# Performance work log

Measured on AMD Instinct MI355X. Metric: run time of the kernel, lower is better.

## Reference

```python
import jax, jax.numpy as jnp
import numpy as np

B, T, DD, NS, V, E, H, L = 8192, 200, 8, 4, 1000, 32, 256, 2


def setup_inputs() -> dict:
    key = jax.random.key(0)
    ks = jax.random.split(key, 10)
    s = 0.05
    dense = jax.random.normal(ks[0], (B, T, DD), jnp.float32)
    sparse = jax.random.randint(ks[1], (B, T, NS), 0, V)
    lengths = jax.random.randint(ks[2], (B,), 1, T + 1)
    emb_tables = jax.random.normal(ks[3], (NS, V, E), jnp.float32) * s
    Wl = jax.random.normal(ks[4], (H, DD + NS * E), jnp.float32) * s
    bl = jnp.zeros((H,), jnp.float32)
    # axis1: 0 = rnn_entry_exit (even t), 1 = rnn_exit_entry (odd t)
    Wih = jax.random.normal(ks[5], (L, 2, H, H), jnp.float32) * s
    Whh = jax.random.normal(ks[6], (L, 2, H, H), jnp.float32) * s
    bih = jnp.zeros((L, 2, H), jnp.float32)
    bhh = jnp.zeros((L, 2, H), jnp.float32)
    Wout = jax.random.normal(ks[7], (1, H), jnp.float32) * s
    bout = jnp.zeros((1,), jnp.float32)
    return dict(dense=dense, sparse=sparse, lengths=lengths, emb_tables=emb_tables,
                Wl=Wl, bl=bl, Wih=Wih, Whh=Whh, bih=bih, bhh=bhh, Wout=Wout, bout=bout)


def reference(dense, sparse, lengths, emb_tables, Wl, bl, Wih, Whh, bih, bhh, Wout, bout):
    # Padded+mask formulation; equivalent to the packed-sequence loop:
    # finished sequences' hidden states are frozen (== being sliced away),
    # and the final frozen h of the top layer is the per-sequence output.
    # Dropout is identity (eval mode); it is never applied in forward anyway.
    mask = jnp.arange(T)[None, :] < lengths[:, None]        # [B, T]
    d_t = jnp.swapaxes(dense, 0, 1)                          # [T, B, DD]
    s_t = jnp.swapaxes(sparse, 0, 1)                         # [T, B, NS]
    m_t = mask.T                                             # [T, B]

    def embed(st):  # [B, NS] -> [B, NS*E], matching torch.cat of per-feature embeddings
        e = jax.vmap(lambda tab, idx: tab[idx], in_axes=(0, 1), out_axes=1)(emb_tables, st)
        return e.reshape(st.shape[0], NS * E)

    def step(h, xs):  # h: [L, B, H]
        t, dt, st, mt = xs
        x = jnp.concatenate([dt, embed(st)], axis=-1)        # [B, DD+NS*E]
        x = jax.nn.relu(x @ Wl.T + bl)                       # [B, H]
        p = t % 2                                            # which cell set this step
        hs = []
        for i in range(L):
            hn = jnp.tanh(x @ Wih[i, p].T + bih[i, p] + h[i] @ Whh[i, p].T + bhh[i, p])
            hi = jnp.where(mt[:, None], hn, h[i])
            hs.append(hi)
            x = hi
        return jnp.stack(hs), None

    h0 = jnp.zeros((L, B, H), dense.dtype)
    hT, _ = jax.lax.scan(step, h0, (jnp.arange(T), d_t, s_t, m_t))
    return jax.nn.sigmoid(hT[-1] @ Wout.T + bout)[:, 0]     # [B]
```

## Files before the change

kernel.cpp:

```cpp
#include <hip/hip_runtime.h>
#include <math.h>


typedef __attribute__((ext_vector_type(8))) short bf16x8;
typedef __attribute__((ext_vector_type(4))) short s16x4;
typedef __attribute__((ext_vector_type(4))) float f32x4;

#define MFMA(a, b, c) __builtin_amdgcn_mfma_f32_16x16x32_bf16((a), (b), (c), 0, 0, 0)

#define T_  200

#define WLP_OFF   0
#define WIHP_OFF  40960
#define WHHP_OFF  (40960 + 262144)
#define BSUM_BYTE_OFF ((40960 + 262144 + 262144) * 2)

#define XCS 168
#define HS  264
#define SM_XCAT 0
#define SM_XPJ  5376
#define SM_H0   (SM_XPJ + 8448)
#define SM_H1A  (SM_H0 + 8448)
#define SM_H1B  (SM_H1A + 8448)
#define SM_BIAS (SM_H1B + 8448)
#define SM_TOT  (SM_BIAS + 2560)

__device__ __forceinline__ short f2bf(float f) {
    unsigned u = __float_as_uint(f);
    u += 0x7fffu + ((u >> 16) & 1u);
    return (short)(u >> 16);
}
__device__ __forceinline__ float bf2f(short s) {
    return __uint_as_float(((unsigned)(unsigned short)s) << 16);
}
__device__ __forceinline__ float tanh_fast(float x) {
    float e = __builtin_amdgcn_exp2f(x * 2.88539008f);
    return 1.0f - 2.0f * __builtin_amdgcn_rcpf(e + 1.0f);
}

__global__ void prep_kernel(const float* __restrict__ Wl,
                            const float* __restrict__ Wih,
                            const float* __restrict__ Whh,
                            const float* __restrict__ bih,
                            const float* __restrict__ bhh,
                            short* __restrict__ wsS,
                            float* __restrict__ bsum) {
    int tid = blockIdx.x * 256 + threadIdx.x;
    if (tid < 5120) {
        int mt = tid / 320, rem = tid % 320;
        int kk = rem / 64, lane = rem % 64;
        int o = mt * 16 + (lane & 15);
        int kb = kk * 32 + (lane >> 4) * 8;
        short* dst = wsS + WLP_OFF + tid * 8;
#pragma unroll
        for (int e = 0; e < 8; e++) {
            int k = kb + e;
            dst[e] = f2bf((k < 136) ? Wl[o * 136 + k] : 0.0f);
        }
    } else if (tid < 5120 + 32768) {
        int jj = tid - 5120;
        int mat = jj / 8192, rem = jj % 8192;
        int lane = rem & 63, kk = (rem >> 6) & 7, mt = rem >> 9;
        int o = mt * 16 + (lane & 15);
        int kb = kk * 32 + (lane >> 4) * 8;
        const float* src = Wih + (mat * 256 + o) * 256;
        short* dst = wsS + WIHP_OFF + mat * 65536 + rem * 8;
#pragma unroll
        for (int e = 0; e < 8; e++) dst[e] = f2bf(src[kb + e]);
    } else if (tid < 5120 + 65536) {
        int jj = tid - 37888;
        int mat = jj / 8192, rem = jj % 8192;
        int lane = rem & 63, kk = (rem >> 6) & 7, mt = rem >> 9;
        int o = mt * 16 + (lane & 15);
        int kb = kk * 32 + (lane >> 4) * 8;
        const float* src = Whh + (mat * 256 + o) * 256;
        short* dst = wsS + WHHP_OFF + mat * 65536 + rem * 8;
#pragma unroll
        for (int e = 0; e < 8; e++) dst[e] = f2bf(src[kb + e]);
    } else if (tid < 5120 + 65536 + 1024) {
        int j = tid - 70656;
        bsum[j] = bih[j] + bhh[j];
    }
}

struct GReg { f32x4 e0, e1, dv; };

__device__ __forceinline__ void gather_load(GReg& g, const float* __restrict__ dense,
                                            const int* __restrict__ sparse,
                                            const float* __restrict__ emb,
                                            int b0, int tt, int tid) {
    int gs = tid >> 4, gf = (tid >> 2) & 3, gq = tid & 3;
    int ix = sparse[(b0 + gs) * (T_ * 4) + tt * 4 + gf];
    const float* ep = emb + gf * 32000 + ix * 32 + gq * 8;
    g.e0 = *(const f32x4*)ep;
    g.e1 = *(const f32x4*)(ep + 4);
    if (tid < 64)
        g.dv = *(const f32x4*)(dense + (b0 + (tid >> 1)) * (T_ * 8) + tt * 8 + (tid & 1) * 4);
}
__device__ __forceinline__ void gather_commit(const GReg& g, short* __restrict__ buf, int tid) {
    int gs = tid >> 4, gf = (tid >> 2) & 3, gq = tid & 3;
    s16x4 w0, w1;
#pragma unroll
    for (int r = 0; r < 4; r++) { w0[r] = f2bf(g.e0[r]); w1[r] = f2bf(g.e1[r]); }
    int off = gs * XCS + 8 + gf * 32 + gq * 8;
    *(s16x4*)(buf + off) = w0;
    *(s16x4*)(buf + off + 4) = w1;
    if (tid < 64) {
        s16x4 wd;
#pragma unroll
        for (int r = 0; r < 4; r++) wd[r] = f2bf(g.dv[r]);
        *(s16x4*)(buf + (tid >> 1) * XCS + (tid & 1) * 4) = wd;
    }
}

__device__ __forceinline__ void phaseA(const short* __restrict__ xcat,
                                       short* __restrict__ xpj,
                                       const short* __restrict__ Wlp,
                                       const float* __restrict__ blS,
                                       int lane, int lrow, int lgrp, int wid) {
    bf16x8 wl[3][2];
#pragma unroll
    for (int j = 0; j < 2; j++) {
        wl[j][0] = *(const bf16x8*)(Wlp + (((wid * 2 + 0) * 5 + j) * 64 + lane) * 8);
        wl[j][1] = *(const bf16x8*)(Wlp + (((wid * 2 + 1) * 5 + j) * 64 + lane) * 8);
    }
    f32x4 xacc[2][2];
#pragma unroll
    for (int mt = 0; mt < 2; mt++) {
        f32x4 bi = *(const f32x4*)(blS + wid * 32 + mt * 16 + lgrp * 4);
        xacc[mt][0] = bi; xacc[mt][1] = bi;
    }
#pragma unroll
    for (int kk = 0; kk < 5; kk++) {
        const int cur = kk % 3;
        if (kk < 3) {
            const int nxt = (kk + 2) % 3;
            wl[nxt][0] = *(const bf16x8*)(Wlp + (((wid * 2 + 0) * 5 + kk + 2) * 64 + lane) * 8);
            wl[nxt][1] = *(const bf16x8*)(Wlp + (((wid * 2 + 1) * 5 + kk + 2) * 64 + lane) * 8);
        }
        bf16x8 bxf[2];
#pragma unroll
        for (int nt = 0; nt < 2; nt++)
            bxf[nt] = *(const bf16x8*)(xcat + (nt * 16 + lrow) * XCS + kk * 32 + lgrp * 8);
#pragma unroll
        for (int mt = 0; mt < 2; mt++)
#pragma unroll
            for (int nt = 0; nt < 2; nt++) xacc[mt][nt] = MFMA(wl[cur][mt], bxf[nt], xacc[mt][nt]);
    }
#pragma unroll
    for (int mt = 0; mt < 2; mt++) {
        int o0 = wid * 32 + mt * 16 + lgrp * 4;
#pragma unroll
        for (int nt = 0; nt < 2; nt++) {
            s16x4 w;
#pragma unroll
            for (int r = 0; r < 4; r++) w[r] = f2bf(fmaxf(xacc[mt][nt][r], 0.0f));
            *(s16x4*)(xpj + (nt * 16 + lrow) * HS + o0) = w;
        }
    }
}

__global__ __launch_bounds__(512, 1) void rnn_kernel(
    const float* __restrict__ dense, const int* __restrict__ sparse,
    const int* __restrict__ lengths, const float* __restrict__ emb,
    const float* __restrict__ bl, const float* __restrict__ Wout,
    const float* __restrict__ bout, const short* __restrict__ wsS,
    const float* __restrict__ bsum, float* __restrict__ out) {
    __shared__ alignas(16) short sm[SM_TOT];
    short* xcat = sm + SM_XCAT;
    short* xpj  = sm + SM_XPJ;
    short* h0p  = sm + SM_H0;
    short* h1a  = sm + SM_H1A;
    short* h1b  = sm + SM_H1B;
    float* blS  = (float*)(sm + SM_BIAS);

    const int tid  = threadIdx.x;
    const int wid  = tid >> 6;
    const int lane = tid & 63;
    const int lrow = lane & 15;
    const int lgrp = lane >> 4;
    const int b0   = blockIdx.x * 32;
    const short* Wlp = wsS + WLP_OFF;

    for (int i = tid; i < SM_BIAS; i += 512) sm[i] = 0;
    for (int i = tid; i < 1280; i += 512)
        blS[i] = (i < 256) ? bl[i] : bsum[i - 256];

    const int len0 = lengths[b0 + lrow];
    const int len1 = lengths[b0 + 16 + lrow];

    __syncthreads();
    { GReg g0; gather_load(g0, dense, sparse, emb, b0, 0, tid); gather_commit(g0, xcat, tid); }
    __syncthreads();
    phaseA(xcat, xpj, Wlp, blS, lane, lrow, lgrp, wid);

    bf16x8 hreg0[2][8];
#pragma unroll
    for (int nt = 0; nt < 2; nt++)
#pragma unroll
        for (int kk = 0; kk < 8; kk++) {
            bf16x8 z;
#pragma unroll
            for (int e = 0; e < 8; e++) z[e] = 0;
            hreg0[nt][kk] = z;
        }
    __syncthreads();

    for (int t = 0; t < T_; t++) {
        const int p = t & 1;
        const bool hasNext = (t + 1 < T_);
        const short* Aih1 = wsS + WIHP_OFF + p * 65536;
        const short* Ahh1 = wsS + WHHP_OFF + p * 65536;
        const short* Aih2 = wsS + WIHP_OFF + (2 + p) * 65536;
        const short* Ahh2 = wsS + WHHP_OFF + (2 + p) * 65536;

        GReg g;
        if (hasNext) gather_load(g, dense, sparse, emb, b0, t + 1, tid);

        {
            bf16x8 wa[3][4];
#pragma unroll
            for (int j = 0; j < 2; j++) {
                wa[j][0] = *(const bf16x8*)(Aih1 + (((wid * 2 + 0) * 8 + j) * 64 + lane) * 8);
                wa[j][1] = *(const bf16x8*)(Aih1 + (((wid * 2 + 1) * 8 + j) * 64 + lane) * 8);
                wa[j][2] = *(const bf16x8*)(Ahh1 + (((wid * 2 + 0) * 8 + j) * 64 + lane) * 8);
                wa[j][3] = *(const bf16x8*)(Ahh1 + (((wid * 2 + 1) * 8 + j) * 64 + lane) * 8);
            }
            f32x4 acc[2][2];
#pragma unroll
            for (int mt = 0; mt < 2; mt++) {
                f32x4 bi = *(const f32x4*)(blS + 256 + p * 256 + wid * 32 + mt * 16 + lgrp * 4);
                acc[mt][0] = bi; acc[mt][1] = bi;
            }
#pragma unroll
            for (int kk = 0; kk < 8; kk++) {
                const int cur = kk % 3;
                if (kk < 6) {
                    const int nxt = (kk + 2) % 3;
                    wa[nxt][0] = *(const bf16x8*)(Aih1 + (((wid * 2 + 0) * 8 + kk + 2) * 64 + lane) * 8);
                    wa[nxt][1] = *(const bf16x8*)(Aih1 + (((wid * 2 + 1) * 8 + kk + 2) * 64 + lane) * 8);
                    wa[nxt][2] = *(const bf16x8*)(Ahh1 + (((wid * 2 + 0) * 8 + kk + 2) * 64 + lane) * 8);
                    wa[nxt][3] = *(const bf16x8*)(Ahh1 + (((wid * 2 + 1) * 8 + kk + 2) * 64 + lane) * 8);
                }
                bf16x8 bxf[2];
#pragma unroll
                for (int nt = 0; nt < 2; nt++)
                    bxf[nt] = *(const bf16x8*)(xpj + (nt * 16 + lrow) * HS + kk * 32 + lgrp * 8);
#pragma unroll
                for (int mt = 0; mt < 2; mt++)
#pragma unroll
                    for (int nt = 0; nt < 2; nt++) {
                        acc[mt][nt] = MFMA(wa[cur][mt], bxf[nt], acc[mt][nt]);
                        acc[mt][nt] = MFMA(wa[cur][2 + mt], hreg0[nt][kk], acc[mt][nt]);
                    }
            }
#pragma unroll
            for (int mt = 0; mt < 2; mt++) {
                int o0 = wid * 32 + mt * 16 + lgrp * 4;
#pragma unroll
                for (int nt = 0; nt < 2; nt++) {
                    s16x4 w;
#pragma unroll
                    for (int r = 0; r < 4; r++) w[r] = f2bf(tanh_fast(acc[mt][nt][r]));
                    int len = nt ? len1 : len0;
                    if (t < len)
                        *(s16x4*)(h0p + (nt * 16 + lrow) * HS + o0) = w;
                }
            }
        }
        if (hasNext) gather_commit(g, xcat, tid);
        __syncthreads();

        {
            const short* h1r = p ? h1b : h1a;
            short* h1w = p ? h1a : h1b;

            bf16x8 wa[3][4];
#pragma unroll
            for (int j = 0; j < 2; j++) {
                wa[j][0] = *(const bf16x8*)(Aih2 + (((wid * 2 + 0) * 8 + j) * 64 + lane) * 8);
                wa[j][1] = *(const bf16x8*)(Aih2 + (((wid * 2 + 1) * 8 + j) * 64 + lane) * 8);
                wa[j][2] = *(const bf16x8*)(Ahh2 + (((wid * 2 + 0) * 8 + j) * 64 + lane) * 8);
                wa[j][3] = *(const bf16x8*)(Ahh2 + (((wid * 2 + 1) * 8 + j) * 64 + lane) * 8);
            }
            f32x4 acc[2][2];
#pragma unroll
            for (int mt = 0; mt < 2; mt++) {
                f32x4 bi = *(const f32x4*)(blS + 256 + (2 + p) * 256 + wid * 32 + mt * 16 + lgrp * 4);
                acc[mt][0] = bi; acc[mt][1] = bi;
            }
#pragma unroll
            for (int kk = 0; kk < 8; kk++) {
                const int cur = kk % 3;
                if (kk < 6) {
                    const int nxt = (kk + 2) % 3;
                    wa[nxt][0] = *(const bf16x8*)(Aih2 + (((wid * 2 + 0) * 8 + kk + 2) * 64 + lane) * 8);
                    wa[nxt][1] = *(const bf16x8*)(Aih2 + (((wid * 2 + 1) * 8 + kk + 2) * 64 + lane) * 8);
                    wa[nxt][2] = *(const bf16x8*)(Ahh2 + (((wid * 2 + 0) * 8 + kk + 2) * 64 + lane) * 8);
                    wa[nxt][3] = *(const bf16x8*)(Ahh2 + (((wid * 2 + 1) * 8 + kk + 2) * 64 + lane) * 8);
                }
                bf16x8 bhf[2];
#pragma unroll
                for (int nt = 0; nt < 2; nt++) {
                    hreg0[nt][kk] = *(const bf16x8*)(h0p + (nt * 16 + lrow) * HS + kk * 32 + lgrp * 8);
                    bhf[nt] = *(const bf16x8*)(h1r + (nt * 16 + lrow) * HS + kk * 32 + lgrp * 8);
                }
#pragma unroll
                for (int mt = 0; mt < 2; mt++)
#pragma unroll
                    for (int nt = 0; nt < 2; nt++) {
                        acc[mt][nt] = MFMA(wa[cur][mt], hreg0[nt][kk], acc[mt][nt]);
                        acc[mt][nt] = MFMA(wa[cur][2 + mt], bhf[nt], acc[mt][nt]);
                    }
            }

            if (hasNext)
                phaseA(xcat, xpj, Wlp, blS, lane, lrow, lgrp, wid);

#pragma unroll
            for (int mt = 0; mt < 2; mt++) {
                int o0 = wid * 32 + mt * 16 + lgrp * 4;
#pragma unroll
                for (int nt = 0; nt < 2; nt++) {
                    int roff = (nt * 16 + lrow) * HS + o0;
                    s16x4 oldv = *(const s16x4*)(h1r + roff);
                    s16x4 w;
#pragma unroll
                    for (int r = 0; r < 4; r++) w[r] = f2bf(tanh_fast(acc[mt][nt][r]));
                    int len = nt ? len1 : len0;
                    *(s16x4*)(h1w + roff) = (t < len) ? w : oldv;
                }
            }
        }
        __syncthreads();
    }

    float* red = (float*)(sm + SM_XPJ);
    if (tid < 256) {
        int s = tid >> 3, part = tid & 7;
        const short* hr = h1a + s * HS + part * 32;
        float sum = 0.0f;
#pragma unroll
        for (int k = 0; k < 32; k++) sum += bf2f(hr[k]) * Wout[part * 32 + k];
        red[s * 8 + part] = sum;
    }
    __syncthreads();
    if (tid < 32) {
        float x = bout[0];
#pragma unroll
        for (int i = 0; i < 8; i++) x += red[tid * 8 + i];
        float e = __builtin_amdgcn_exp2f(x * 1.44269504f);
        out[b0 + tid] = 1.0f - __builtin_amdgcn_rcpf(1.0f + e);
    }
}

extern "C" void kernel_launch(void* const* d_in, const int* in_sizes, int n_in,
                              void* d_out, int out_size, void* d_ws, size_t ws_size,
                              hipStream_t stream) {
    const float* dense   = (const float*)d_in[0];
    const int*   sparse  = (const int*)d_in[1];
    const int*   lengths = (const int*)d_in[2];
    const float* emb     = (const float*)d_in[3];
    const float* Wl      = (const float*)d_in[4];
    const float* bl      = (const float*)d_in[5];
    const float* Wih     = (const float*)d_in[6];
    const float* Whh     = (const float*)d_in[7];
    const float* bih     = (const float*)d_in[8];
    const float* bhh     = (const float*)d_in[9];
    const float* Wout    = (const float*)d_in[10];
    const float* bout    = (const float*)d_in[11];

    short* wsS  = (short*)d_ws;
    float* bsum = (float*)((char*)d_ws + BSUM_BYTE_OFF);

    prep_kernel<<<280, 256, 0, stream>>>(Wl, Wih, Whh, bih, bhh, wsS, bsum);
    rnn_kernel<<<256, 512, 0, stream>>>(dense, sparse, lengths, emb, bl, Wout, bout,
                                        wsS, bsum, (float*)d_out);
}
```

Before: 1.205 ms.

## Software-pipeline weight loads across RNN layers and steps with rotating register slots

Restructures each time step into a template function whose weight-fragment loads run three chunks ahead in a 4-slot rotating register buffer, continuing across layer-1, layer-2, the next step's input projection, and the next step's layer-1 weights. The loop is unrolled by 4 so slot offsets are compile-time constants. The input projection moves after the layer-2 output write, and barriers become explicit lgkmcnt waits plus s_barrier with a sched_barrier. The goal is to hide the global/L2 weight-load latency at layer and step boundaries, at the cost of more register pressure and a longer unrolled body.

```diff
diff --git a/kernel.cpp b/kernel.cpp
--- a/kernel.cpp
+++ b/kernel.cpp
@@ -24,6 +24,10 @@
 #define SM_H1B  (SM_H1A + 8448)
 #define SM_BIAS (SM_H1B + 8448)
 #define SM_TOT  (SM_BIAS + 2560)
+
+#define LGKM0()    asm volatile("s_waitcnt lgkmcnt(0)" ::: "memory")
+#define BARRIER()  do { LGKM0(); __builtin_amdgcn_s_barrier(); \
+                        __builtin_amdgcn_sched_barrier(0); } while (0)
 
 __device__ __forceinline__ short f2bf(float f) {
     unsigned u = __float_as_uint(f);
@@ -113,39 +117,69 @@
     }
 }
 
-__device__ __forceinline__ void phaseA(const short* __restrict__ xcat,
-                                       short* __restrict__ xpj,
-                                       const short* __restrict__ Wlp,
-                                       const float* __restrict__ blS,
-                                       int lane, int lrow, int lgrp, int wid) {
-    bf16x8 wl[3][2];
-#pragma unroll
-    for (int j = 0; j < 2; j++) {
-        wl[j][0] = *(const bf16x8*)(Wlp + (((wid * 2 + 0) * 5 + j) * 64 + lane) * 8);
-        wl[j][1] = *(const bf16x8*)(Wlp + (((wid * 2 + 1) * 5 + j) * 64 + lane) * 8);
-    }
-    f32x4 xacc[2][2];
+__device__ __forceinline__ void load_chunk(bf16x8 (&wa)[4][4], int slot,
+                                           const short* A, const short* B,
+                                           int kk, int wid, int lane) {
+    wa[slot][0] = *(const bf16x8*)(A + (((wid * 2 + 0) * 8 + kk) * 64 + lane) * 8);
+    wa[slot][1] = *(const bf16x8*)(A + (((wid * 2 + 1) * 8 + kk) * 64 + lane) * 8);
+    wa[slot][2] = *(const bf16x8*)(B + (((wid * 2 + 0) * 8 + kk) * 64 + lane) * 8);
+    wa[slot][3] = *(const bf16x8*)(B + (((wid * 2 + 1) * 8 + kk) * 64 + lane) * 8);
+}
+__device__ __forceinline__ void load_wl(bf16x8 (&wa)[4][4], int slot,
+                                        const short* Wlp, int kk, int wid, int lane) {
+    wa[slot][0] = *(const bf16x8*)(Wlp + (((wid * 2 + 0) * 5 + kk) * 64 + lane) * 8);
+    wa[slot][1] = *(const bf16x8*)(Wlp + (((wid * 2 + 1) * 5 + kk) * 64 + lane) * 8);
+}
+
+template<int P, int OFF, bool LAST>
+__device__ __forceinline__ void rnn_step(
+    int t,
+    const float* __restrict__ dense, const int* __restrict__ sparse,
+    const float* __restrict__ emb, const short* __restrict__ wsS,
+    const float* __restrict__ blS,
+    short* __restrict__ xcat, short* __restrict__ xpj, short* __restrict__ h0p,
+    short* __restrict__ h1a, short* __restrict__ h1b,
+    bf16x8 (&wa)[4][4], bf16x8 (&hreg0)[2][8],
+    int lane, int lrow, int lgrp, int wid, int len0, int len1, int b0, int tid)
+{
+    const short* Aih1 = wsS + WIHP_OFF + P * 65536;
+    const short* Ahh1 = wsS + WHHP_OFF + P * 65536;
+    const short* Aih2 = wsS + WIHP_OFF + (2 + P) * 65536;
+    const short* Ahh2 = wsS + WHHP_OFF + (2 + P) * 65536;
+    const short* AihN = wsS + WIHP_OFF + (P ^ 1) * 65536;
+    const short* AhhN = wsS + WHHP_OFF + (P ^ 1) * 65536;
+    const short* Wlp  = wsS + WLP_OFF;
+
+    GReg g;
+    if (!LAST) gather_load(g, dense, sparse, emb, b0, t + 1, tid);
+
+    f32x4 acc[2][2];
+
 #pragma unroll
     for (int mt = 0; mt < 2; mt++) {
-        f32x4 bi = *(const f32x4*)(blS + wid * 32 + mt * 16 + lgrp * 4);
-        xacc[mt][0] = bi; xacc[mt][1] = bi;
-    }
-#pragma unroll
-    for (int kk = 0; kk < 5; kk++) {
-        const int cur = kk % 3;
-        if (kk < 3) {
-            const int nxt = (kk + 2) % 3;
-            wl[nxt][0] = *(const bf16x8*)(Wlp + (((wid * 2 + 0) * 5 + kk + 2) * 64 + lane) * 8);
-            wl[nxt][1] = *(const bf16x8*)(Wlp + (((wid * 2 + 1) * 5 + kk + 2) * 64 + lane) * 8);
-        }
+        f32x4 bi = *(const f32x4*)(blS + 256 + P * 256 + wid * 32 + mt * 16 + lgrp * 4);
+        acc[mt][0] = bi; acc[mt][1] = bi;
+    }
+#pragma unroll
+    for (int u = 0; u < 8; u++) {
+        {
+            const int v = u + 3;
+            const int vs = (v + OFF) & 3;
+            if (v < 8) load_chunk(wa, vs, Aih1, Ahh1, v, wid, lane);
+            else       load_chunk(wa, vs, Aih2, Ahh2, v - 8, wid, lane);
+        }
+        const int slot = (u + OFF) & 3;
         bf16x8 bxf[2];
 #pragma unroll
         for (int nt = 0; nt < 2; nt++)
-            bxf[nt] = *(const bf16x8*)(xcat + (nt * 16 + lrow) * XCS + kk * 32 + lgrp * 8);
+            bxf[nt] = *(const bf16x8*)(xpj + (nt * 16 + lrow) * HS + u * 32 + lgrp * 8);
 #pragma unroll
         for (int mt = 0; mt < 2; mt++)
 #pragma unroll
-            for (int nt = 0; nt < 2; nt++) xacc[mt][nt] = MFMA(wl[cur][mt], bxf[nt], xacc[mt][nt]);
+            for (int nt = 0; nt < 2; nt++) {
+                acc[mt][nt] = MFMA(wa[slot][mt], bxf[nt], acc[mt][nt]);
+                acc[mt][nt] = MFMA(wa[slot][2 + mt], hreg0[nt][u], acc[mt][nt]);
+            }
     }
 #pragma unroll
     for (int mt = 0; mt < 2; mt++) {
@@ -154,10 +188,100 @@
         for (int nt = 0; nt < 2; nt++) {
             s16x4 w;
 #pragma unroll
-            for (int r = 0; r < 4; r++) w[r] = f2bf(fmaxf(xacc[mt][nt][r], 0.0f));
-            *(s16x4*)(xpj + (nt * 16 + lrow) * HS + o0) = w;
-        }
-    }
+            for (int r = 0; r < 4; r++) w[r] = f2bf(tanh_fast(acc[mt][nt][r]));
+            int len = nt ? len1 : len0;
+            if (t < len)
+                *(s16x4*)(h0p + (nt * 16 + lrow) * HS + o0) = w;
+        }
+    }
+    if (!LAST) gather_commit(g, xcat, tid);
+    BARRIER();
+
+    const short* h1r = P ? h1b : h1a;
+    short* h1w = P ? h1a : h1b;
+#pragma unroll
+    for (int mt = 0; mt < 2; mt++) {
+        f32x4 bi = *(const f32x4*)(blS + 256 + (2 + P) * 256 + wid * 32 + mt * 16 + lgrp * 4);
+        acc[mt][0] = bi; acc[mt][1] = bi;
+    }
+#pragma unroll
+    for (int u = 8; u < 16; u++) {
+        {
+            const int v = u + 3;
+            const int vs = (v + OFF) & 3;
+            if (v < 16)      load_chunk(wa, vs, Aih2, Ahh2, v - 8, wid, lane);
+            else if (!LAST)  load_wl(wa, vs, Wlp, v - 16, wid, lane);
+        }
+        const int slot = (u + OFF) & 3;
+        const int kk = u - 8;
+        bf16x8 bhf[2];
+#pragma unroll
+        for (int nt = 0; nt < 2; nt++) {
+            hreg0[nt][kk] = *(const bf16x8*)(h0p + (nt * 16 + lrow) * HS + kk * 32 + lgrp * 8);
+            bhf[nt] = *(const bf16x8*)(h1r + (nt * 16 + lrow) * HS + kk * 32 + lgrp * 8);
+        }
+#pragma unroll
+        for (int mt = 0; mt < 2; mt++)
+#pragma unroll
+            for (int nt = 0; nt < 2; nt++) {
+                acc[mt][nt] = MFMA(wa[slot][mt], hreg0[nt][kk], acc[mt][nt]);
+                acc[mt][nt] = MFMA(wa[slot][2 + mt], bhf[nt], acc[mt][nt]);
+            }
+    }
+#pragma unroll
+    for (int mt = 0; mt < 2; mt++) {
+        int o0 = wid * 32 + mt * 16 + lgrp * 4;
+#pragma unroll
+        for (int nt = 0; nt < 2; nt++) {
+            int roff = (nt * 16 + lrow) * HS + o0;
+            s16x4 oldv = *(const s16x4*)(h1r + roff);
+            s16x4 w;
+#pragma unroll
+            for (int r = 0; r < 4; r++) w[r] = f2bf(tanh_fast(acc[mt][nt][r]));
+            int len = nt ? len1 : len0;
+            *(s16x4*)(h1w + roff) = (t < len) ? w : oldv;
+        }
+    }
+
+    if (!LAST) {
+#pragma unroll
+        for (int mt = 0; mt < 2; mt++) {
+            f32x4 bi = *(const f32x4*)(blS + wid * 32 + mt * 16 + lgrp * 4);
+            acc[mt][0] = bi; acc[mt][1] = bi;
+        }
+#pragma unroll
+        for (int u = 16; u < 21; u++) {
+            {
+                const int v = u + 3;
+                const int vs = (v + OFF) & 3;
+                if (v < 21) load_wl(wa, vs, Wlp, v - 16, wid, lane);
+                else        load_chunk(wa, vs, AihN, AhhN, v - 21, wid, lane);
+            }
+            const int slot = (u + OFF) & 3;
+            const int kk = u - 16;
+            bf16x8 bxf[2];
+#pragma unroll
+            for (int nt = 0; nt < 2; nt++)
+                bxf[nt] = *(const bf16x8*)(xcat + (nt * 16 + lrow) * XCS + kk * 32 + lgrp * 8);
+#pragma unroll
+            for (int mt = 0; mt < 2; mt++)
+#pragma unroll
+                for (int nt = 0; nt < 2; nt++)
+                    acc[mt][nt] = MFMA(wa[slot][mt], bxf[nt], acc[mt][nt]);
+        }
+#pragma unroll
+        for (int mt = 0; mt < 2; mt++) {
+            int o0 = wid * 32 + mt * 16 + lgrp * 4;
+#pragma unroll
+            for (int nt = 0; nt < 2; nt++) {
+                s16x4 w;
+#pragma unroll
+                for (int r = 0; r < 4; r++) w[r] = f2bf(fmaxf(acc[mt][nt][r], 0.0f));
+                *(s16x4*)(xpj + (nt * 16 + lrow) * HS + o0) = w;
+            }
+        }
+    }
+    BARRIER();
 }
 
 __global__ __launch_bounds__(512, 1) void rnn_kernel(
@@ -192,8 +316,42 @@
     __syncthreads();
     { GReg g0; gather_load(g0, dense, sparse, emb, b0, 0, tid); gather_commit(g0, xcat, tid); }
     __syncthreads();
-    phaseA(xcat, xpj, Wlp, blS, lane, lrow, lgrp, wid);
-
+
+    {
+        f32x4 xacc[2][2];
+#pragma unroll
+        for (int mt = 0; mt < 2; mt++) {
+            f32x4 bi = *(const f32x4*)(blS + wid * 32 + mt * 16 + lgrp * 4);
+            xacc[mt][0] = bi; xacc[mt][1] = bi;
+        }
+#pragma unroll
+        for (int kk = 0; kk < 5; kk++) {
+            bf16x8 wl0 = *(const bf16x8*)(Wlp + (((wid * 2 + 0) * 5 + kk) * 64 + lane) * 8);
+            bf16x8 wl1 = *(const bf16x8*)(Wlp + (((wid * 2 + 1) * 5 + kk) * 64 + lane) * 8);
+            bf16x8 bxf[2];
+#pragma unroll
+            for (int nt = 0; nt < 2; nt++)
+                bxf[nt] = *(const bf16x8*)(xcat + (nt * 16 + lrow) * XCS + kk * 32 + lgrp * 8);
+#pragma unroll
+            for (int nt = 0; nt < 2; nt++) {
+                xacc[0][nt] = MFMA(wl0, bxf[nt], xacc[0][nt]);
+                xacc[1][nt] = MFMA(wl1, bxf[nt], xacc[1][nt]);
+            }
+        }
+#pragma unroll
+        for (int mt = 0; mt < 2; mt++) {
+            int o0 = wid * 32 + mt * 16 + lgrp * 4;
+#pragma unroll
+            for (int nt = 0; nt < 2; nt++) {
+                s16x4 w;
+#pragma unroll
+                for (int r = 0; r < 4; r++) w[r] = f2bf(fmaxf(xacc[mt][nt][r], 0.0f));
+                *(s16x4*)(xpj + (nt * 16 + lrow) * HS + o0) = w;
+            }
+        }
+    }
+
+    bf16x8 wa[4][4];
     bf16x8 hreg0[2][8];
 #pragma unroll
     for (int nt = 0; nt < 2; nt++)
@@ -204,136 +362,28 @@
             for (int e = 0; e < 8; e++) z[e] = 0;
             hreg0[nt][kk] = z;
         }
-    __syncthreads();
-
-    for (int t = 0; t < T_; t++) {
-        const int p = t & 1;
-        const bool hasNext = (t + 1 < T_);
-        const short* Aih1 = wsS + WIHP_OFF + p * 65536;
-        const short* Ahh1 = wsS + WHHP_OFF + p * 65536;
-        const short* Aih2 = wsS + WIHP_OFF + (2 + p) * 65536;
-        const short* Ahh2 = wsS + WHHP_OFF + (2 + p) * 65536;
-
-        GReg g;
-        if (hasNext) gather_load(g, dense, sparse, emb, b0, t + 1, tid);
-
-        {
-            bf16x8 wa[3][4];
-#pragma unroll
-            for (int j = 0; j < 2; j++) {
-                wa[j][0] = *(const bf16x8*)(Aih1 + (((wid * 2 + 0) * 8 + j) * 64 + lane) * 8);
-                wa[j][1] = *(const bf16x8*)(Aih1 + (((wid * 2 + 1) * 8 + j) * 64 + lane) * 8);
-                wa[j][2] = *(const bf16x8*)(Ahh1 + (((wid * 2 + 0) * 8 + j) * 64 + lane) * 8);
-                wa[j][3] = *(const bf16x8*)(Ahh1 + (((wid * 2 + 1) * 8 + j) * 64 + lane) * 8);
-            }
-            f32x4 acc[2][2];
-#pragma unroll
-            for (int mt = 0; mt < 2; mt++) {
-                f32x4 bi = *(const f32x4*)(blS + 256 + p * 256 + wid * 32 + mt * 16 + lgrp * 4);
-                acc[mt][0] = bi; acc[mt][1] = bi;
-            }
-#pragma unroll
-            for (int kk = 0; kk < 8; kk++) {
-                const int cur = kk % 3;
-                if (kk < 6) {
-                    const int nxt = (kk + 2) % 3;
-                    wa[nxt][0] = *(const bf16x8*)(Aih1 + (((wid * 2 + 0) * 8 + kk + 2) * 64 + lane) * 8);
-                    wa[nxt][1] = *(const bf16x8*)(Aih1 + (((wid * 2 + 1) * 8 + kk + 2) * 64 + lane) * 8);
-                    wa[nxt][2] = *(const bf16x8*)(Ahh1 + (((wid * 2 + 0) * 8 + kk + 2) * 64 + lane) * 8);
-                    wa[nxt][3] = *(const bf16x8*)(Ahh1 + (((wid * 2 + 1) * 8 + kk + 2) * 64 + lane) * 8);
-                }
-                bf16x8 bxf[2];
-#pragma unroll
-                for (int nt = 0; nt < 2; nt++)
-                    bxf[nt] = *(const bf16x8*)(xpj + (nt * 16 + lrow) * HS + kk * 32 + lgrp * 8);
-#pragma unroll
-                for (int mt = 0; mt < 2; mt++)
-#pragma unroll
-                    for (int nt = 0; nt < 2; nt++) {
-                        acc[mt][nt] = MFMA(wa[cur][mt], bxf[nt], acc[mt][nt]);
-                        acc[mt][nt] = MFMA(wa[cur][2 + mt], hreg0[nt][kk], acc[mt][nt]);
-                    }
-            }
-#pragma unroll
-            for (int mt = 0; mt < 2; mt++) {
-                int o0 = wid * 32 + mt * 16 + lgrp * 4;
-#pragma unroll
-                for (int nt = 0; nt < 2; nt++) {
-                    s16x4 w;
-#pragma unroll
-                    for (int r = 0; r < 4; r++) w[r] = f2bf(tanh_fast(acc[mt][nt][r]));
-                    int len = nt ? len1 : len0;
-                    if (t < len)
-                        *(s16x4*)(h0p + (nt * 16 + lrow) * HS + o0) = w;
-                }
-            }
-        }
-        if (hasNext) gather_commit(g, xcat, tid);
-        __syncthreads();
-
-        {
-            const short* h1r = p ? h1b : h1a;
-            short* h1w = p ? h1a : h1b;
-
-            bf16x8 wa[3][4];
-#pragma unroll
-            for (int j = 0; j < 2; j++) {
-                wa[j][0] = *(const bf16x8*)(Aih2 + (((wid * 2 + 0) * 8 + j) * 64 + lane) * 8);
-                wa[j][1] = *(const bf16x8*)(Aih2 + (((wid * 2 + 1) * 8 + j) * 64 + lane) * 8);
-                wa[j][2] = *(const bf16x8*)(Ahh2 + (((wid * 2 + 0) * 8 + j) * 64 + lane) * 8);
-                wa[j][3] = *(const bf16x8*)(Ahh2 + (((wid * 2 + 1) * 8 + j) * 64 + lane) * 8);
-            }
-            f32x4 acc[2][2];
-#pragma unroll
-            for (int mt = 0; mt < 2; mt++) {
-                f32x4 bi = *(const f32x4*)(blS + 256 + (2 + p) * 256 + wid * 32 + mt * 16 + lgrp * 4);
-                acc[mt][0] = bi; acc[mt][1] = bi;
-            }
-#pragma unroll
-            for (int kk = 0; kk < 8; kk++) {
-                const int cur = kk % 3;
-                if (kk < 6) {
-                    const int nxt = (kk + 2) % 3;
-                    wa[nxt][0] = *(const bf16x8*)(Aih2 + (((wid * 2 + 0) * 8 + kk + 2) * 64 + lane) * 8);
-                    wa[nxt][1] = *(const bf16x8*)(Aih2 + (((wid * 2 + 1) * 8 + kk + 2) * 64 + lane) * 8);
-                    wa[nxt][2] = *(const bf16x8*)(Ahh2 + (((wid * 2 + 0) * 8 + kk + 2) * 64 + lane) * 8);
-                    wa[nxt][3] = *(const bf16x8*)(Ahh2 + (((wid * 2 + 1) * 8 + kk + 2) * 64 + lane) * 8);
-                }
-                bf16x8 bhf[2];
-#pragma unroll
-                for (int nt = 0; nt < 2; nt++) {
-                    hreg0[nt][kk] = *(const bf16x8*)(h0p + (nt * 16 + lrow) * HS + kk * 32 + lgrp * 8);
-                    bhf[nt] = *(const bf16x8*)(h1r + (nt * 16 + lrow) * HS + kk * 32 + lgrp * 8);
-                }
-#pragma unroll
-                for (int mt = 0; mt < 2; mt++)
-#pragma unroll
-                    for (int nt = 0; nt < 2; nt++) {
-                        acc[mt][nt] = MFMA(wa[cur][mt], hreg0[nt][kk], acc[mt][nt]);
-                        acc[mt][nt] = MFMA(wa[cur][2 + mt], bhf[nt], acc[mt][nt]);
-                    }
-            }
-
-            if (hasNext)
-                phaseA(xcat, xpj, Wlp, blS, lane, lrow, lgrp, wid);
-
-#pragma unroll
-            for (int mt = 0; mt < 2; mt++) {
-                int o0 = wid * 32 + mt * 16 + lgrp * 4;
-#pragma unroll
-                for (int nt = 0; nt < 2; nt++) {
-                    int roff = (nt * 16 + lrow) * HS + o0;
-                    s16x4 oldv = *(const s16x4*)(h1r + roff);
-                    s16x4 w;
-#pragma unroll
-                    for (int r = 0; r < 4; r++) w[r] = f2bf(tanh_fast(acc[mt][nt][r]));
-                    int len = nt ? len1 : len0;
-                    *(s16x4*)(h1w + roff) = (t < len) ? w : oldv;
-                }
-            }
-        }
-        __syncthreads();
-    }
+
+    load_chunk(wa, 0, wsS + WIHP_OFF, wsS + WHHP_OFF, 0, wid, lane);
+    load_chunk(wa, 1, wsS + WIHP_OFF, wsS + WHHP_OFF, 1, wid, lane);
+    load_chunk(wa, 2, wsS + WIHP_OFF, wsS + WHHP_OFF, 2, wid, lane);
+    BARRIER();
+
+#define STEP(PP, OO, LL, tt) \
+    rnn_step<PP, OO, LL>(tt, dense, sparse, emb, wsS, blS, xcat, xpj, h0p, \
+                         h1a, h1b, wa, hreg0, lane, lrow, lgrp, wid, \
+                         len0, len1, b0, tid)
+
+    for (int tb = 0; tb < T_ - 4; tb += 4) {
+        STEP(0, 0, false, tb);
+        STEP(1, 1, false, tb + 1);
+        STEP(0, 2, false, tb + 2);
+        STEP(1, 3, false, tb + 3);
+    }
+    STEP(0, 0, false, T_ - 4);
+    STEP(1, 1, false, T_ - 3);
+    STEP(0, 2, false, T_ - 2);
+    STEP(1, 3, true,  T_ - 1);
+#undef STEP
 
     float* red = (float*)(sm + SM_XPJ);
     if (tid < 256) {
```

After: 4.569 ms. 3.79x slower.

## Software-pipeline weight prefetch across RNN phases and move gather two steps ahead

Applied to the files above, without the earlier changes.

Restructures the per-timestep loop so weight-fragment prefetches run continuously across phase boundaries. The tail of layer-1 prefetches layer-2 weights, the tail of layer-2 prefetches the input-projection weights, and the projection prefetches the next step's layer-1 weights. This removes the cold-start global loads at the beginning of each phase. The embedding/dense gather for step t+2 is issued after the projection instead of at the top of the loop, giving it more time in flight. The cost is more live registers, an inlined projection, and a reorder where the projection now runs after the layer-2 epilogue.

```diff
diff --git a/kernel.cpp b/kernel.cpp
--- a/kernel.cpp
+++ b/kernel.cpp
@@ -113,51 +113,17 @@
     }
 }
 
-__device__ __forceinline__ void phaseA(const short* __restrict__ xcat,
-                                       short* __restrict__ xpj,
-                                       const short* __restrict__ Wlp,
-                                       const float* __restrict__ blS,
-                                       int lane, int lrow, int lgrp, int wid) {
-    bf16x8 wl[3][2];
-#pragma unroll
-    for (int j = 0; j < 2; j++) {
-        wl[j][0] = *(const bf16x8*)(Wlp + (((wid * 2 + 0) * 5 + j) * 64 + lane) * 8);
-        wl[j][1] = *(const bf16x8*)(Wlp + (((wid * 2 + 1) * 5 + j) * 64 + lane) * 8);
-    }
-    f32x4 xacc[2][2];
-#pragma unroll
-    for (int mt = 0; mt < 2; mt++) {
-        f32x4 bi = *(const f32x4*)(blS + wid * 32 + mt * 16 + lgrp * 4);
-        xacc[mt][0] = bi; xacc[mt][1] = bi;
-    }
-#pragma unroll
-    for (int kk = 0; kk < 5; kk++) {
-        const int cur = kk % 3;
-        if (kk < 3) {
-            const int nxt = (kk + 2) % 3;
-            wl[nxt][0] = *(const bf16x8*)(Wlp + (((wid * 2 + 0) * 5 + kk + 2) * 64 + lane) * 8);
-            wl[nxt][1] = *(const bf16x8*)(Wlp + (((wid * 2 + 1) * 5 + kk + 2) * 64 + lane) * 8);
-        }
-        bf16x8 bxf[2];
-#pragma unroll
-        for (int nt = 0; nt < 2; nt++)
-            bxf[nt] = *(const bf16x8*)(xcat + (nt * 16 + lrow) * XCS + kk * 32 + lgrp * 8);
-#pragma unroll
-        for (int mt = 0; mt < 2; mt++)
-#pragma unroll
-            for (int nt = 0; nt < 2; nt++) xacc[mt][nt] = MFMA(wl[cur][mt], bxf[nt], xacc[mt][nt]);
-    }
-#pragma unroll
-    for (int mt = 0; mt < 2; mt++) {
-        int o0 = wid * 32 + mt * 16 + lgrp * 4;
-#pragma unroll
-        for (int nt = 0; nt < 2; nt++) {
-            s16x4 w;
-#pragma unroll
-            for (int r = 0; r < 4; r++) w[r] = f2bf(fmaxf(xacc[mt][nt][r], 0.0f));
-            *(s16x4*)(xpj + (nt * 16 + lrow) * HS + o0) = w;
-        }
-    }
+__device__ __forceinline__ void load_c4(bf16x8 (&d)[4], const short* A, const short* B,
+                                        int kk, int wid, int lane) {
+    d[0] = *(const bf16x8*)(A + (((wid * 2 + 0) * 8 + kk) * 64 + lane) * 8);
+    d[1] = *(const bf16x8*)(A + (((wid * 2 + 1) * 8 + kk) * 64 + lane) * 8);
+    d[2] = *(const bf16x8*)(B + (((wid * 2 + 0) * 8 + kk) * 64 + lane) * 8);
+    d[3] = *(const bf16x8*)(B + (((wid * 2 + 1) * 8 + kk) * 64 + lane) * 8);
+}
+__device__ __forceinline__ void load_wl2(bf16x8& d0, bf16x8& d1,
+                                         const short* Wlp, int kk, int wid, int lane) {
+    d0 = *(const bf16x8*)(Wlp + (((wid * 2 + 0) * 5 + kk) * 64 + lane) * 8);
+    d1 = *(const bf16x8*)(Wlp + (((wid * 2 + 1) * 5 + kk) * 64 + lane) * 8);
 }
 
 __global__ __launch_bounds__(512, 1) void rnn_kernel(
@@ -192,8 +158,43 @@
     __syncthreads();
     { GReg g0; gather_load(g0, dense, sparse, emb, b0, 0, tid); gather_commit(g0, xcat, tid); }
     __syncthreads();
-    phaseA(xcat, xpj, Wlp, blS, lane, lrow, lgrp, wid);
-
+
+    {
+        f32x4 xacc[2][2];
+#pragma unroll
+        for (int mt = 0; mt < 2; mt++) {
+            f32x4 bi = *(const f32x4*)(blS + wid * 32 + mt * 16 + lgrp * 4);
+            xacc[mt][0] = bi; xacc[mt][1] = bi;
+        }
+#pragma unroll
+        for (int kk = 0; kk < 5; kk++) {
+            bf16x8 wl0, wl1;
+            load_wl2(wl0, wl1, Wlp, kk, wid, lane);
+            bf16x8 bxf[2];
+#pragma unroll
+            for (int nt = 0; nt < 2; nt++)
+                bxf[nt] = *(const bf16x8*)(xcat + (nt * 16 + lrow) * XCS + kk * 32 + lgrp * 8);
+#pragma unroll
+            for (int nt = 0; nt < 2; nt++) {
+                xacc[0][nt] = MFMA(wl0, bxf[nt], xacc[0][nt]);
+                xacc[1][nt] = MFMA(wl1, bxf[nt], xacc[1][nt]);
+            }
+        }
+#pragma unroll
+        for (int mt = 0; mt < 2; mt++) {
+            int o0 = wid * 32 + mt * 16 + lgrp * 4;
+#pragma unroll
+            for (int nt = 0; nt < 2; nt++) {
+                s16x4 w;
+#pragma unroll
+                for (int r = 0; r < 4; r++) w[r] = f2bf(fmaxf(xacc[mt][nt][r], 0.0f));
+                *(s16x4*)(xpj + (nt * 16 + lrow) * HS + o0) = w;
+            }
+        }
+    }
+
+    bf16x8 wa[3][4];
+    bf16x8 wnext[4];
     bf16x8 hreg0[2][8];
 #pragma unroll
     for (int nt = 0; nt < 2; nt++)
@@ -204,7 +205,14 @@
             for (int e = 0; e < 8; e++) z[e] = 0;
             hreg0[nt][kk] = z;
         }
+
+    load_c4(wa[0], wsS + WIHP_OFF, wsS + WHHP_OFF, 0, wid, lane);
+    load_c4(wa[1], wsS + WIHP_OFF, wsS + WHHP_OFF, 1, wid, lane);
+    GReg g;
+    gather_load(g, dense, sparse, emb, b0, 1, tid);
     __syncthreads();
+
+    f32x4 acc[2][2];
 
     for (int t = 0; t < T_; t++) {
         const int p = t & 1;
@@ -213,46 +221,124 @@
         const short* Ahh1 = wsS + WHHP_OFF + p * 65536;
         const short* Aih2 = wsS + WIHP_OFF + (2 + p) * 65536;
         const short* Ahh2 = wsS + WHHP_OFF + (2 + p) * 65536;
-
-        GReg g;
-        if (hasNext) gather_load(g, dense, sparse, emb, b0, t + 1, tid);
-
-        {
-            bf16x8 wa[3][4];
-#pragma unroll
-            for (int j = 0; j < 2; j++) {
-                wa[j][0] = *(const bf16x8*)(Aih1 + (((wid * 2 + 0) * 8 + j) * 64 + lane) * 8);
-                wa[j][1] = *(const bf16x8*)(Aih1 + (((wid * 2 + 1) * 8 + j) * 64 + lane) * 8);
-                wa[j][2] = *(const bf16x8*)(Ahh1 + (((wid * 2 + 0) * 8 + j) * 64 + lane) * 8);
-                wa[j][3] = *(const bf16x8*)(Ahh1 + (((wid * 2 + 1) * 8 + j) * 64 + lane) * 8);
-            }
-            f32x4 acc[2][2];
+        const short* AihN = wsS + WIHP_OFF + (p ^ 1) * 65536;
+        const short* AhhN = wsS + WHHP_OFF + (p ^ 1) * 65536;
+
+#pragma unroll
+        for (int mt = 0; mt < 2; mt++) {
+            f32x4 bi = *(const f32x4*)(blS + 256 + p * 256 + wid * 32 + mt * 16 + lgrp * 4);
+            acc[mt][0] = bi; acc[mt][1] = bi;
+        }
+#pragma unroll
+        for (int kk = 0; kk < 8; kk++) {
+            if (kk <= 5)      load_c4(wa[(kk + 2) % 3], Aih1, Ahh1, kk + 2, wid, lane);
+            else if (kk == 6) load_c4(wnext, Aih2, Ahh2, 0, wid, lane);
+            else              load_c4(wa[2], Aih2, Ahh2, 1, wid, lane);
+            const int s = kk % 3;
+            bf16x8 bxf[2];
+#pragma unroll
+            for (int nt = 0; nt < 2; nt++)
+                bxf[nt] = *(const bf16x8*)(xpj + (nt * 16 + lrow) * HS + kk * 32 + lgrp * 8);
+#pragma unroll
+            for (int mt = 0; mt < 2; mt++)
+#pragma unroll
+                for (int nt = 0; nt < 2; nt++) {
+                    acc[mt][nt] = MFMA(wa[s][mt], bxf[nt], acc[mt][nt]);
+                    acc[mt][nt] = MFMA(wa[s][2 + mt], hreg0[nt][kk], acc[mt][nt]);
+                }
+        }
+#pragma unroll
+        for (int mt = 0; mt < 2; mt++) {
+            int o0 = wid * 32 + mt * 16 + lgrp * 4;
+#pragma unroll
+            for (int nt = 0; nt < 2; nt++) {
+                s16x4 w;
+#pragma unroll
+                for (int r = 0; r < 4; r++) w[r] = f2bf(tanh_fast(acc[mt][nt][r]));
+                int len = nt ? len1 : len0;
+                if (t < len)
+                    *(s16x4*)(h0p + (nt * 16 + lrow) * HS + o0) = w;
+            }
+        }
+        if (hasNext) gather_commit(g, xcat, tid);
+        __syncthreads();
+
+        const short* h1r = p ? h1b : h1a;
+        short* h1w = p ? h1a : h1b;
+#pragma unroll
+        for (int mt = 0; mt < 2; mt++) {
+            f32x4 bi = *(const f32x4*)(blS + 256 + (2 + p) * 256 + wid * 32 + mt * 16 + lgrp * 4);
+            acc[mt][0] = bi; acc[mt][1] = bi;
+        }
+#pragma unroll
+        for (int kk = 0; kk < 8; kk++) {
+            if (kk <= 5)      load_c4(wa[kk % 3], Aih2, Ahh2, kk + 2, wid, lane);
+            else if (kk == 6) { if (hasNext) load_wl2(wnext[0], wnext[1], Wlp, 0, wid, lane); }
+            else              { if (hasNext) load_wl2(wnext[2], wnext[3], Wlp, 1, wid, lane); }
+            bf16x8 bhf[2];
+#pragma unroll
+            for (int nt = 0; nt < 2; nt++) {
+                hreg0[nt][kk] = *(const bf16x8*)(h0p + (nt * 16 + lrow) * HS + kk * 32 + lgrp * 8);
+                bhf[nt] = *(const bf16x8*)(h1r + (nt * 16 + lrow) * HS + kk * 32 + lgrp * 8);
+            }
+            if (kk == 0) {
+#pragma unroll
+                for (int mt = 0; mt < 2; mt++)
+#pragma unroll
+                    for (int nt = 0; nt < 2; nt++) {
+                        acc[mt][nt] = MFMA(wnext[mt], hreg0[nt][0], acc[mt][nt]);
+                        acc[mt][nt] = MFMA(wnext[2 + mt], bhf[nt], acc[mt][nt]);
+                    }
+            } else {
+                const int s = (kk + 1) % 3;
+#pragma unroll
+                for (int mt = 0; mt < 2; mt++)
+#pragma unroll
+                    for (int nt = 0; nt < 2; nt++) {
+                        acc[mt][nt] = MFMA(wa[s][mt], hreg0[nt][kk], acc[mt][nt]);
+                        acc[mt][nt] = MFMA(wa[s][2 + mt], bhf[nt], acc[mt][nt]);
+                    }
+            }
+        }
+#pragma unroll
+        for (int mt = 0; mt < 2; mt++) {
+            int o0 = wid * 32 + mt * 16 + lgrp * 4;
+#pragma unroll
+            for (int nt = 0; nt < 2; nt++) {
+                int roff = (nt * 16 + lrow) * HS + o0;
+                s16x4 oldv = *(const s16x4*)(h1r + roff);
+                s16x4 w;
+#pragma unroll
+                for (int r = 0; r < 4; r++) w[r] = f2bf(tanh_fast(acc[mt][nt][r]));
+                int len = nt ? len1 : len0;
+                *(s16x4*)(h1w + roff) = (t < len) ? w : oldv;
+            }
+        }
+
+        if (hasNext) {
 #pragma unroll
             for (int mt = 0; mt < 2; mt++) {
-                f32x4 bi = *(const f32x4*)(blS + 256 + p * 256 + wid * 32 + mt * 16 + lgrp * 4);
+                f32x4 bi = *(const f32x4*)(blS + wid * 32 + mt * 16 + lgrp * 4);
                 acc[mt][0] = bi; acc[mt][1] = bi;
             }
 #pragma unroll
-            for (int kk = 0; kk < 8; kk++) {
-                const int cur = kk % 3;
-                if (kk < 6) {
-                    const int nxt = (kk + 2) % 3;
-                    wa[nxt][0] = *(const bf16x8*)(Aih1 + (((wid * 2 + 0) * 8 + kk + 2) * 64 + lane) * 8);
-                    wa[nxt][1] = *(const bf16x8*)(Aih1 + (((wid * 2 + 1) * 8 + kk + 2) * 64 + lane) * 8);
-                    wa[nxt][2] = *(const bf16x8*)(Ahh1 + (((wid * 2 + 0) * 8 + kk + 2) * 64 + lane) * 8);
-                    wa[nxt][3] = *(const bf16x8*)(Ahh1 + (((wid * 2 + 1) * 8 + kk + 2) * 64 + lane) * 8);
+            for (int kk = 0; kk < 5; kk++) {
+                if (kk <= 2)      load_wl2(wa[kk][0], wa[kk][1], Wlp, kk + 2, wid, lane);
+                else if (kk == 3) load_c4(wa[0], AihN, AhhN, 0, wid, lane);
+                else              load_c4(wa[1], AihN, AhhN, 1, wid, lane);
+                bf16x8 w0, w1;
+                if (kk == 0)      { w0 = wnext[0]; w1 = wnext[1]; }
+                else if (kk == 1) { w0 = wnext[2]; w1 = wnext[3]; }
+                else              { w0 = wa[kk - 2][0]; w1 = wa[kk - 2][1]; }
+                bf16x8 bxf[2];
+#pragma unroll
+                for (int nt = 0; nt < 2; nt++)
+                    bxf[nt] = *(const bf16x8*)(xcat + (nt * 16 + lrow) * XCS + kk * 32 + lgrp * 8);
+#pragma unroll
+                for (int nt = 0; nt < 2; nt++) {
+                    acc[0][nt] = MFMA(w0, bxf[nt], acc[0][nt]);
+                    acc[1][nt] = MFMA(w1, bxf[nt], acc[1][nt]);
                 }
-                bf16x8 bxf[2];
-#pragma unroll
-                for (int nt = 0; nt < 2; nt++)
-                    bxf[nt] = *(const bf16x8*)(xpj + (nt * 16 + lrow) * HS + kk * 32 + lgrp * 8);
-#pragma unroll
-                for (int mt = 0; mt < 2; mt++)
-#pragma unroll
-                    for (int nt = 0; nt < 2; nt++) {
-                        acc[mt][nt] = MFMA(wa[cur][mt], bxf[nt], acc[mt][nt]);
-                        acc[mt][nt] = MFMA(wa[cur][2 + mt], hreg0[nt][kk], acc[mt][nt]);
-                    }
             }
 #pragma unroll
             for (int mt = 0; mt < 2; mt++) {
@@ -261,76 +347,12 @@
                 for (int nt = 0; nt < 2; nt++) {
                     s16x4 w;
 #pragma unroll
-                    for (int r = 0; r < 4; r++) w[r] = f2bf(tanh_fast(acc[mt][nt][r]));
-                    int len = nt ? len1 : len0;
-                    if (t < len)
-                        *(s16x4*)(h0p + (nt * 16 + lrow) * HS + o0) = w;
+                    for (int r = 0; r < 4; r++) w[r] = f2bf(fmaxf(acc[mt][nt][r], 0.0f));
+                    *(s16x4*)(xpj + (nt * 16 + lrow) * HS + o0) = w;
                 }
             }
-        }
-        if (hasNext) gather_commit(g, xcat, tid);
-        __syncthreads();
-
-        {
-            const short* h1r = p ? h1b : h1a;
-            short* h1w = p ? h1a : h1b;
-
-            bf16x8 wa[3][4];
-#pragma unroll
-            for (int j = 0; j < 2; j++) {
-                wa[j][0] = *(const bf16x8*)(Aih2 + (((wid * 2 + 0) * 8 + j) * 64 + lane) * 8);
-                wa[j][1] = *(const bf16x8*)(Aih2 + (((wid * 2 + 1) * 8 + j) * 64 + lane) * 8);
-                wa[j][2] = *(const bf16x8*)(Ahh2 + (((wid * 2 + 0) * 8 + j) * 64 + lane) * 8);
-                wa[j][3] = *(const bf16x8*)(Ahh2 + (((wid * 2 + 1) * 8 + j) * 64 + lane) * 8);
-            }
-            f32x4 acc[2][2];
-#pragma unroll
-            for (int mt = 0; mt < 2; mt++) {
-                f32x4 bi = *(const f32x4*)(blS + 256 + (2 + p) * 256 + wid * 32 + mt * 16 + lgrp * 4);
-                acc[mt][0] = bi; acc[mt][1] = bi;
-            }
-#pragma unroll
-            for (int kk = 0; kk < 8; kk++) {
-                const int cur = kk % 3;
-                if (kk < 6) {
-                    const int nxt = (kk + 2) % 3;
-                    wa[nxt][0] = *(const bf16x8*)(Aih2 + (((wid * 2 + 0) * 8 + kk + 2) * 64 + lane) * 8);
-                    wa[nxt][1] = *(const bf16x8*)(Aih2 + (((wid * 2 + 1) * 8 + kk + 2) * 64 + lane) * 8);
-                    wa[nxt][2] = *(const bf16x8*)(Ahh2 + (((wid * 2 + 0) * 8 + kk + 2) * 64 + lane) * 8);
-                    wa[nxt][3] = *(const bf16x8*)(Ahh2 + (((wid * 2 + 1) * 8 + kk + 2) * 64 + lane) * 8);
-                }
-                bf16x8 bhf[2];
-#pragma unroll
-                for (int nt = 0; nt < 2; nt++) {
-                    hreg0[nt][kk] = *(const bf16x8*)(h0p + (nt * 16 + lrow) * HS + kk * 32 + lgrp * 8);
-                    bhf[nt] = *(const bf16x8*)(h1r + (nt * 16 + lrow) * HS + kk * 32 + lgrp * 8);
-                }
-#pragma unroll
-                for (int mt = 0; mt < 2; mt++)
-#pragma unroll
-                    for (int nt = 0; nt < 2; nt++) {
-                        acc[mt][nt] = MFMA(wa[cur][mt], hreg0[nt][kk], acc[mt][nt]);
-                        acc[mt][nt] = MFMA(wa[cur][2 + mt], bhf[nt], acc[mt][nt]);
-                    }
-            }
-
-            if (hasNext)
-                phaseA(xcat, xpj, Wlp, blS, lane, lrow, lgrp, wid);
-
-#pragma unroll
-            for (int mt = 0; mt < 2; mt++) {
-                int o0 = wid * 32 + mt * 16 + lgrp * 4;
-#pragma unroll
-                for (int nt = 0; nt < 2; nt++) {
-                    int roff = (nt * 16 + lrow) * HS + o0;
-                    s16x4 oldv = *(const s16x4*)(h1r + roff);
-                    s16x4 w;
-#pragma unroll
-                    for (int r = 0; r < 4; r++) w[r] = f2bf(tanh_fast(acc[mt][nt][r]));
-                    int len = nt ? len1 : len0;
-                    *(s16x4*)(h1w + roff) = (t < len) ? w : oldv;
-                }
-            }
+            if (t + 2 < T_)
+                gather_load(g, dense, sparse, emb, b0, t + 2, tid);
         }
         __syncthreads();
     }
```

New measurement: 1.157 ms (median of 2 runs). -4.0%, faster.
